# Performance work log

Hardware: AMD Instinct MI355X
Metric: run time of the kernel (lower is better)

## Reference

```python
import jax, jax.numpy as jnp
import numpy as np

EPS = 1e-06
ITERS = 10


def _dilate(x):
    # 3x3 max-pool, stride 1, same padding; torch pads max_pool with -inf
    return jax.lax.reduce_window(x, -jnp.inf, jax.lax.max,
                                 (1, 1, 3, 3), (1, 1, 1, 1), 'SAME')


def _erode(x):
    return -_dilate(-x)


def _soft_skeletonize(img, iters=ITERS):
    skel = jnp.zeros_like(img)
    for _ in range(iters):
        opened = _dilate(_erode(img))
        delta = jax.nn.relu(img - opened)
        skel = skel + jax.nn.relu(delta - skel)
        img = _erode(img)
    return skel


def setup_inputs() -> dict:
    key = jax.random.key(0)
    k1, k2 = jax.random.split(key)
    pred_prob = jax.random.normal(k1, (32, 1, 1024, 1024), dtype=jnp.float32)
    gt_onehot = jax.random.uniform(k2, (32, 1, 1024, 1024), dtype=jnp.float32)
    return {"pred_prob": pred_prob, "gt_onehot": gt_onehot}


def reference(pred_prob, gt_onehot):
    # binary branch: C == 1, logits -> sigmoid
    p = jax.nn.sigmoid(pred_prob)
    skel_pred = _soft_skeletonize(p, ITERS)
    skel_gt = _soft_skeletonize(gt_onehot, ITERS)
    tprec = jnp.sum(skel_pred * gt_onehot, axis=(2, 3)) / (jnp.sum(skel_pred, axis=(2, 3)) + EPS)
    tsens = jnp.sum(skel_gt * p, axis=(2, 3)) / (jnp.sum(skel_gt, axis=(2, 3)) + EPS)
    cldice = 2 * tprec * tsens / (tprec + tsens + EPS)
    return 1.0 - jnp.mean(cldice)
```

## Files before the change

### kernel.cpp

```cpp
#include <hip/hip_runtime.h>
#include <math.h>


typedef unsigned int u32;
typedef _Float16 h2 __attribute__((ext_vector_type(2)));

#define STRD 52
#define BB   0x7BFF7BFFu
#define NB   0xFBFFFBFFu

__device__ __forceinline__ u32 ab(u32 hi, u32 lo) {
  return __builtin_amdgcn_alignbit(hi, lo, 16);
}
__device__ __forceinline__ u32 bcu(h2 x) { return __builtin_bit_cast(u32, x); }
__device__ __forceinline__ h2  bch(u32 x) { return __builtin_bit_cast(h2, x); }
__device__ __forceinline__ u32 pmin(u32 a, u32 b) {
  return bcu(__builtin_elementwise_min(bch(a), bch(b)));
}
__device__ __forceinline__ u32 pmax(u32 a, u32 b) {
  return bcu(__builtin_elementwise_max(bch(a), bch(b)));
}
__device__ __forceinline__ u32 pmin3(u32 a, u32 b, u32 c) { return pmin(pmin(a, b), c); }
__device__ __forceinline__ u32 pmax3(u32 a, u32 b, u32 c) { return pmax(pmax(a, b), c); }
__device__ __forceinline__ u32 skup(u32 sk, u32 im, u32 op) {
  h2 d = bch(im) - bch(op);
  return bcu(__builtin_elementwise_max(bch(sk), d));
}
__device__ __forceinline__ float sigmoidf_(float x) {
  return 1.0f / (1.0f + __expf(-x));
}

__device__ __forceinline__ void load12(const u32* __restrict__ p,
                                       u32* __restrict__ r) {
  uint4 a = *(const uint4*)p;
  uint4 b = *(const uint4*)(p + 4);
  uint4 c = *(const uint4*)(p + 8);
  r[0]=a.x; r[1]=a.y; r[2]=a.z; r[3]=a.w;
  r[4]=b.x; r[5]=b.y; r[6]=b.z; r[7]=b.w;
  r[8]=c.x; r[9]=c.y; r[10]=c.z; r[11]=c.w;
}

__device__ __forceinline__ void store12(u32* __restrict__ q,
                                        const u32* __restrict__ r) {
  *(uint4*)(q)     = make_uint4(r[0], r[1], r[2],  r[3]);
  *(uint4*)(q + 4) = make_uint4(r[4], r[5], r[6],  r[7]);
  *(uint4*)(q + 8) = make_uint4(r[8], r[9], r[10], r[11]);
}

__device__ __forceinline__ void hrow12(const u32* __restrict__ v,
                                       u32 hl, u32 hr,
                                       u32* __restrict__ o) {
  u32 m0 = ab(v[0], hl);
  #pragma unroll
  for (int i = 0; i < 12; ++i) {
    u32 m1 = (i < 11) ? ab(v[i + 1], v[i]) : ab(hr, v[11]);
    o[i] = pmin3(m0, v[i], m1);
    m0 = m1;
  }
}

template <bool FIRST>
__device__ __forceinline__ void erode_compute(
    const u32* __restrict__ E,
    int as3, int eoff, int pu, int pd, bool c0, bool c3,
    u32* __restrict__ e0, u32* __restrict__ e1, u32* __restrict__ e2)
{
  const u32* pr = E + (as3 - 1) * STRD + eoff;
  u32 rT[12], rB[12];
  load12(pr, rT);
  if (FIRST) {
    load12(pr + STRD,     e0);
    load12(pr + 2 * STRD, e1);
    load12(pr + 3 * STRD, e2);
  }
  load12(pr + 4 * STRD, rB);
  u32 t[12], v0[12], v1[12], v2[12];
  #pragma unroll
  for (int i = 0; i < 12; ++i) t[i]  = pmin(e0[i], e1[i]);
  #pragma unroll
  for (int i = 0; i < 12; ++i) v0[i] = pmin(rT[i], t[i]);
  #pragma unroll
  for (int i = 0; i < 12; ++i) v1[i] = pmin(t[i], e2[i]);
  #pragma unroll
  for (int i = 0; i < 12; ++i) v2[i] = pmin(e1[i], pmin(e2[i], rB[i]));
  u32 hl0 = (u32)__builtin_amdgcn_ds_bpermute(pu, (int)v0[11]);
  u32 hr0 = (u32)__builtin_amdgcn_ds_bpermute(pd, (int)v0[0]);
  u32 hl1 = (u32)__builtin_amdgcn_ds_bpermute(pu, (int)v1[11]);
  u32 hr1 = (u32)__builtin_amdgcn_ds_bpermute(pd, (int)v1[0]);
  u32 hl2 = (u32)__builtin_amdgcn_ds_bpermute(pu, (int)v2[11]);
  u32 hr2 = (u32)__builtin_amdgcn_ds_bpermute(pd, (int)v2[0]);
  hl0 = c0 ? BB : hl0;  hr0 = c3 ? BB : hr0;
  hl1 = c0 ? BB : hl1;  hr1 = c3 ? BB : hr1;
  hl2 = c0 ? BB : hl2;  hr2 = c3 ? BB : hr2;
  hrow12(v0, hl0, hr0, e0);
  hrow12(v1, hl1, hr1, e1);
  hrow12(v2, hl2, hr2, e2);
}

__device__ __forceinline__ void erode_store(
    u32* __restrict__ E, int as3, int eoff,
    const u32* __restrict__ e0, const u32* __restrict__ e1,
    const u32* __restrict__ e2)
{
  u32* qw = E + as3 * STRD + eoff;
  store12(qw,            e0);
  store12(qw + STRD,     e1);
  store12(qw + 2 * STRD, e2);
}

__device__ __forceinline__ void dilate_phase(
    const u32* __restrict__ E, const u32* __restrict__ NBR,
    int dr, int db, bool bu, bool bd, bool lfix, bool rfix,
    u32* __restrict__ img, u32* __restrict__ sk)
{
  const u32* pm = bu ? (E + (dr - 1) * STRD + db) : (NBR + db);
  const u32* pc = E + dr * STRD + db;
  const u32* pp = bd ? (E + (dr + 1) * STRD + db) : (NBR + db);
  u32 vm[21];
  #pragma unroll
  for (int j = 0; j < 6; ++j) {
    uint4 x = *(const uint4*)(pm + 4 * j);
    uint4 y = *(const uint4*)(pc + 4 * j);
    uint4 z = *(const uint4*)(pp + 4 * j);
    u32 xs[4] = {x.x, x.y, x.z, x.w};
    u32 ys[4] = {y.x, y.y, y.z, y.w};
    u32 zs[4] = {z.x, z.y, z.z, z.w};
    #pragma unroll
    for (int k = 0; k < 4; ++k) {
      int i = 4 * j + k;
      if (i >= 3 && i <= 20) vm[i] = pmax3(xs[k], ys[k], zs[k]);
    }
  }
  if (lfix) vm[3]  = (vm[3]  & 0x0000FFFFu) | 0xFBFF0000u;
  if (rfix) vm[20] = (vm[20] & 0xFFFF0000u) | 0x0000FBFFu;
  u32 m0 = ab(vm[4], vm[3]);
  #pragma unroll
  for (int j = 0; j < 4; ++j) {
    const uint4 y = *(const uint4*)(pc + 4 + 4 * j);
    const u32 yk[4] = {y.x, y.y, y.z, y.w};
    #pragma unroll
    for (int k = 0; k < 4; ++k) {
      const int i = 4 * j + k;
      u32 m1 = ab(vm[i + 5], vm[i + 4]);
      u32 op = pmax3(m0, vm[i + 4], m1);
      m0 = m1;
      sk[i] = skup(sk[i], img[i], op);
      img[i] = yk[k];
    }
  }
}

__global__ __launch_bounds__(256, 5) void skel_tile_kernel(
    const float* __restrict__ pred, const float* __restrict__ gt,
    float* __restrict__ sums)
{
  __shared__ __align__(16) u32 L[STRD * 97];
  u32* const E = L;
  const u32* const NBR = L + STRD * 96;

  const int tile = blockIdx.x;
  const int b    = blockIdx.y;
  const int s    = blockIdx.z;
  const int txI = tile & 15, tyI = tile >> 4;
  const int x0 = txI * 64 - 16, y0 = tyI * 64 - 16;
  const int t  = threadIdx.x;
  const size_t base = (size_t)b << 20;
  const float* __restrict__ src  = s ? gt   : pred;
  const float* __restrict__ osrc = s ? pred : gt;

  for (int i = t; i < STRD; i += 256) L[STRD * 96 + i] = NB;

  for (int i = t; i < 86 * 12; i += 256) {
    int ci = i % 12, row = i / 12 + 5;
    int gy = y0 + row, gx0 = x0 + ci * 8;
    uint4 hv;
    if ((unsigned)gy < 1024u && gx0 >= 0 && gx0 + 8 <= 1024) {
      const size_t g = base + (size_t)gy * 1024 + gx0;
      const float4 f0 = *(const float4*)&src[g];
      const float4 f1 = *(const float4*)&src[g + 4];
      float ff[8] = {f0.x, f0.y, f0.z, f0.w, f1.x, f1.y, f1.z, f1.w};
      u32 d[4];
      #pragma unroll
      for (int e = 0; e < 4; ++e) {
        float a = ff[2 * e], bb2 = ff[2 * e + 1];
        if (s == 0) { a = sigmoidf_(a); bb2 = sigmoidf_(bb2); }
        h2 p; p[0] = (_Float16)a; p[1] = (_Float16)bb2;
        d[e] = bcu(p);
      }
      hv = make_uint4(d[0], d[1], d[2], d[3]);
    } else {
      u32 d[4];
      #pragma unroll
      for (int e = 0; e < 4; ++e) {
        float va = 65504.0f, vb = 65504.0f;
        int gxa = gx0 + 2 * e, gxb = gxa + 1;
        if ((unsigned)gy < 1024u && (unsigned)gxa < 1024u) {
          va = src[base + (size_t)gy * 1024 + gxa];
          if (s == 0) va = sigmoidf_(va);
        }
        if ((unsigned)gy < 1024u && (unsigned)gxb < 1024u) {
          vb = src[base + (size_t)gy * 1024 + gxb];
          if (s == 0) vb = sigmoidf_(vb);
        }
        h2 p; p[0] = (_Float16)va; p[1] = (_Float16)vb;
        d[e] = bcu(p);
      }
      hv = make_uint4(d[0], d[1], d[2], d[3]);
    }
    *(uint4*)&E[row * STRD + ci * 4] = hv;
  }
  __syncthreads();

  const int lane = t & 63, wid = t >> 6;

  const int seg = t >> 2, ec = t & 3;
  const int as3 = 3 * seg;
  const bool c0 = (ec == 0), c3 = (ec == 3);
  const int pu = ((lane - 1) & 63) * 4;
  const int pd = ((lane + 1) & 63) * 4;
  const int eoff = 12 * ec;

  const int q  = wid - 2;
  const int dr = 16 + lane;
  const int db = 4 + 16 * q;
  const int gyD = y0 + dr;
  const bool bu = (gyD >= 1), bd = (gyD <= 1022);
  const bool lfix = (q == 0) && (txI == 0);
  const bool rfix = (q == 1) && (txI == 15);

  u32 st[36];
  u32* const e0 = st;
  u32* const e1 = st + 12;
  u32* const e2 = st + 24;
  u32* const img = st;
  u32* const sk  = st + 16;

  const bool a0 = !(as3 + 2 < 6 || as3 > 89);
  if (wid < 2) {
    if (a0) erode_compute<true>(E, as3, eoff, pu, pd, c0, c3, e0, e1, e2);
  } else {
    #pragma unroll
    for (int i = 0; i < 16; ++i) sk[i] = 0;
    const u32* p = E + dr * STRD + db;
    #pragma unroll
    for (int i = 0; i < 4; ++i) {
      uint4 v = *(const uint4*)(p + 4 + 4 * i);
      img[4*i] = v.x; img[4*i+1] = v.y; img[4*i+2] = v.z; img[4*i+3] = v.w;
    }
  }
  __syncthreads();
  if (wid < 2 && a0) erode_store(E, as3, eoff, e0, e1, e2);
  __syncthreads();

  #pragma unroll 1
  for (int it = 1; it <= 10; ++it) {
    const bool act = (it < 10) && !(as3 + 2 < 6 + it || as3 > 89 - it);
    if (wid < 2) {
      if (act) erode_compute<false>(E, as3, eoff, pu, pd, c0, c3, e0, e1, e2);
    } else {
      dilate_phase(E, NBR, dr, db, bu, bd, lfix, rfix, img, sk);
    }
    __syncthreads();
    if (wid < 2 && act) erode_store(E, as3, eoff, e0, e1, e2);
    __syncthreads();
  }

  float s0 = 0.f, s1 = 0.f;
  if (wid >= 2) {
    const int gxb = x0 + 2 * db + 8;
    const size_t g = base + (size_t)gyD * 1024 + gxb;
    #pragma unroll
    for (int v4i = 0; v4i < 8; ++v4i) {
      const float4 f = *(const float4*)&osrc[g + 4 * v4i];
      float o0 = f.x, o1 = f.y, o2 = f.z, o3 = f.w;
      if (s == 1) {
        o0 = sigmoidf_(o0); o1 = sigmoidf_(o1);
        o2 = sigmoidf_(o2); o3 = sigmoidf_(o3);
      }
      h2 qa = bch(sk[2 * v4i]);
      h2 qb = bch(sk[2 * v4i + 1]);
      float a0 = (float)qa[0], a1 = (float)qa[1];
      float a2 = (float)qb[0], a3 = (float)qb[1];
      s0 += a0 * o0 + a1 * o1 + a2 * o2 + a3 * o3;
      s1 += a0 + a1 + a2 + a3;
    }
  }
  for (int off = 32; off >= 1; off >>= 1) {
    s0 += __shfl_down(s0, off, 64);
    s1 += __shfl_down(s1, off, 64);
  }
  float* red = (float*)L;
  if (lane == 0) { red[wid * 2] = s0; red[wid * 2 + 1] = s1; }
  __syncthreads();
  if (t == 0) {
    atomicAdd(&sums[(s * 32 + b) * 2 + 0], red[4] + red[6]);
    atomicAdd(&sums[(s * 32 + b) * 2 + 1], red[5] + red[7]);
  }
}

__global__ void finalize_kernel(const float* __restrict__ sums,
                                float* __restrict__ out)
{
  const int t = threadIdx.x;
  float cl = 0.f;
  if (t < 32) {
    float pn = sums[t * 2 + 0],        pd = sums[t * 2 + 1];
    float sn = sums[(32 + t) * 2 + 0], sd = sums[(32 + t) * 2 + 1];
    float tprec = pn / (pd + 1e-6f);
    float tsens = sn / (sd + 1e-6f);
    cl = 2.f * tprec * tsens / (tprec + tsens + 1e-6f);
  }
  for (int off = 32; off >= 1; off >>= 1) cl += __shfl_down(cl, off, 64);
  if (t == 0) out[0] = 1.f - cl / 32.f;
}

extern "C" void kernel_launch(void* const* d_in, const int* in_sizes, int n_in,
                              void* d_out, int out_size, void* d_ws, size_t ws_size,
                              hipStream_t stream) {
  const float* pred = (const float*)d_in[0];
  const float* gt   = (const float*)d_in[1];
  float* sums = (float*)d_ws;
  hipMemsetAsync(sums, 0, 128 * sizeof(float), stream);
  dim3 grid(256, 32, 2);
  skel_tile_kernel<<<grid, dim3(256), 0, stream>>>(pred, gt, sums);
  finalize_kernel<<<1, 64, 0, stream>>>(sums, (float*)d_out);
}
```

Baseline: 647.0 us.

## Split erosion across three wavefronts with two rows per thread, peel final dilate

Adds a third erosion wavefront (320 threads per block) so each erode thread handles 2 rows instead of 3. This shortens the per-iteration erosion critical path that the dilate wavefronts wait on at each barrier. The final dilate pass is peeled out of the loop so the last iteration skips two barriers. The cost is more threads per block and possibly fewer resident blocks, and the reduction indices shift to the new dilate wavefronts.

After: 808.9 us. +25.0%, slower.

```diff
diff --git a/kernel.cpp b/kernel.cpp
--- a/kernel.cpp
+++ b/kernel.cpp
@@ -62,50 +62,41 @@
 template <bool FIRST>
 __device__ __forceinline__ void erode_compute(
     const u32* __restrict__ E,
-    int as3, int eoff, int pu, int pd, bool c0, bool c3,
-    u32* __restrict__ e0, u32* __restrict__ e1, u32* __restrict__ e2)
-{
-  const u32* pr = E + (as3 - 1) * STRD + eoff;
+    int as2, int eoff, int pu, int pd, bool c0, bool c3,
+    u32* __restrict__ e0, u32* __restrict__ e1)
+{
+  const u32* pr = E + (as2 - 1) * STRD + eoff;
   u32 rT[12], rB[12];
   load12(pr, rT);
   if (FIRST) {
     load12(pr + STRD,     e0);
     load12(pr + 2 * STRD, e1);
-    load12(pr + 3 * STRD, e2);
-  }
-  load12(pr + 4 * STRD, rB);
-  u32 t[12], v0[12], v1[12], v2[12];
-  #pragma unroll
-  for (int i = 0; i < 12; ++i) t[i]  = pmin(e0[i], e1[i]);
-  #pragma unroll
-  for (int i = 0; i < 12; ++i) v0[i] = pmin(rT[i], t[i]);
-  #pragma unroll
-  for (int i = 0; i < 12; ++i) v1[i] = pmin(t[i], e2[i]);
-  #pragma unroll
-  for (int i = 0; i < 12; ++i) v2[i] = pmin(e1[i], pmin(e2[i], rB[i]));
+  }
+  load12(pr + 3 * STRD, rB);
+  u32 tt[12], v0[12], v1[12];
+  #pragma unroll
+  for (int i = 0; i < 12; ++i) tt[i] = pmin(e0[i], e1[i]);
+  #pragma unroll
+  for (int i = 0; i < 12; ++i) v0[i] = pmin(rT[i], tt[i]);
+  #pragma unroll
+  for (int i = 0; i < 12; ++i) v1[i] = pmin(tt[i], rB[i]);
   u32 hl0 = (u32)__builtin_amdgcn_ds_bpermute(pu, (int)v0[11]);
   u32 hr0 = (u32)__builtin_amdgcn_ds_bpermute(pd, (int)v0[0]);
   u32 hl1 = (u32)__builtin_amdgcn_ds_bpermute(pu, (int)v1[11]);
   u32 hr1 = (u32)__builtin_amdgcn_ds_bpermute(pd, (int)v1[0]);
-  u32 hl2 = (u32)__builtin_amdgcn_ds_bpermute(pu, (int)v2[11]);
-  u32 hr2 = (u32)__builtin_amdgcn_ds_bpermute(pd, (int)v2[0]);
   hl0 = c0 ? BB : hl0;  hr0 = c3 ? BB : hr0;
   hl1 = c0 ? BB : hl1;  hr1 = c3 ? BB : hr1;
-  hl2 = c0 ? BB : hl2;  hr2 = c3 ? BB : hr2;
   hrow12(v0, hl0, hr0, e0);
   hrow12(v1, hl1, hr1, e1);
-  hrow12(v2, hl2, hr2, e2);
 }
 
 __device__ __forceinline__ void erode_store(
-    u32* __restrict__ E, int as3, int eoff,
-    const u32* __restrict__ e0, const u32* __restrict__ e1,
-    const u32* __restrict__ e2)
-{
-  u32* qw = E + as3 * STRD + eoff;
-  store12(qw,            e0);
-  store12(qw + STRD,     e1);
-  store12(qw + 2 * STRD, e2);
+    u32* __restrict__ E, int as2, int eoff,
+    const u32* __restrict__ e0, const u32* __restrict__ e1)
+{
+  u32* qw = E + as2 * STRD + eoff;
+  store12(qw,        e0);
+  store12(qw + STRD, e1);
 }
 
 __device__ __forceinline__ void dilate_phase(
@@ -150,7 +141,7 @@
   }
 }
 
-__global__ __launch_bounds__(256, 5) void skel_tile_kernel(
+__global__ __launch_bounds__(320, 5) void skel_tile_kernel(
     const float* __restrict__ pred, const float* __restrict__ gt,
     float* __restrict__ sums)
 {
@@ -168,9 +159,9 @@
   const float* __restrict__ src  = s ? gt   : pred;
   const float* __restrict__ osrc = s ? pred : gt;
 
-  for (int i = t; i < STRD; i += 256) L[STRD * 96 + i] = NB;
-
-  for (int i = t; i < 86 * 12; i += 256) {
+  for (int i = t; i < STRD; i += 320) L[STRD * 96 + i] = NB;
+
+  for (int i = t; i < 86 * 12; i += 320) {
     int ci = i % 12, row = i / 12 + 5;
     int gy = y0 + row, gx0 = x0 + ci * 8;
     uint4 hv;
@@ -214,13 +205,13 @@
   const int lane = t & 63, wid = t >> 6;
 
   const int seg = t >> 2, ec = t & 3;
-  const int as3 = 3 * seg;
+  const int as2 = 2 * seg;
   const bool c0 = (ec == 0), c3 = (ec == 3);
   const int pu = ((lane - 1) & 63) * 4;
   const int pd = ((lane + 1) & 63) * 4;
   const int eoff = 12 * ec;
 
-  const int q  = wid - 2;
+  const int q  = wid - 3;
   const int dr = 16 + lane;
   const int db = 4 + 16 * q;
   const int gyD = y0 + dr;
@@ -228,16 +219,15 @@
   const bool lfix = (q == 0) && (txI == 0);
   const bool rfix = (q == 1) && (txI == 15);
 
-  u32 st[36];
+  u32 st[32];
   u32* const e0 = st;
   u32* const e1 = st + 12;
-  u32* const e2 = st + 24;
   u32* const img = st;
   u32* const sk  = st + 16;
 
-  const bool a0 = !(as3 + 2 < 6 || as3 > 89);
-  if (wid < 2) {
-    if (a0) erode_compute<true>(E, as3, eoff, pu, pd, c0, c3, e0, e1, e2);
+  const bool a0 = !(as2 + 1 < 6 || as2 > 89);
+  if (wid < 3) {
+    if (a0) erode_compute<true>(E, as2, eoff, pu, pd, c0, c3, e0, e1);
   } else {
     #pragma unroll
     for (int i = 0; i < 16; ++i) sk[i] = 0;
@@ -249,24 +239,28 @@
     }
   }
   __syncthreads();
-  if (wid < 2 && a0) erode_store(E, as3, eoff, e0, e1, e2);
+  if (wid < 3 && a0) erode_store(E, as2, eoff, e0, e1);
   __syncthreads();
 
   #pragma unroll 1
-  for (int it = 1; it <= 10; ++it) {
-    const bool act = (it < 10) && !(as3 + 2 < 6 + it || as3 > 89 - it);
-    if (wid < 2) {
-      if (act) erode_compute<false>(E, as3, eoff, pu, pd, c0, c3, e0, e1, e2);
+  for (int it = 1; it <= 9; ++it) {
+    const bool act = !(as2 + 1 < 6 + it || as2 > 89 - it);
+    if (wid < 3) {
+      if (act) erode_compute<false>(E, as2, eoff, pu, pd, c0, c3, e0, e1);
     } else {
       dilate_phase(E, NBR, dr, db, bu, bd, lfix, rfix, img, sk);
     }
     __syncthreads();
-    if (wid < 2 && act) erode_store(E, as3, eoff, e0, e1, e2);
+    if (wid < 3 && act) erode_store(E, as2, eoff, e0, e1);
     __syncthreads();
   }
 
+  if (wid >= 3) {
+    dilate_phase(E, NBR, dr, db, bu, bd, lfix, rfix, img, sk);
+  }
+
   float s0 = 0.f, s1 = 0.f;
-  if (wid >= 2) {
+  if (wid >= 3) {
     const int gxb = x0 + 2 * db + 8;
     const size_t g = base + (size_t)gyD * 1024 + gxb;
     #pragma unroll
@@ -293,8 +287,8 @@
   if (lane == 0) { red[wid * 2] = s0; red[wid * 2 + 1] = s1; }
   __syncthreads();
   if (t == 0) {
-    atomicAdd(&sums[(s * 32 + b) * 2 + 0], red[4] + red[6]);
-    atomicAdd(&sums[(s * 32 + b) * 2 + 1], red[5] + red[7]);
+    atomicAdd(&sums[(s * 32 + b) * 2 + 0], red[6] + red[8]);
+    atomicAdd(&sums[(s * 32 + b) * 2 + 1], red[7] + red[9]);
   }
 }
 
@@ -322,6 +316,6 @@
   float* sums = (float*)d_ws;
   hipMemsetAsync(sums, 0, 128 * sizeof(float), stream);
   dim3 grid(256, 32, 2);
-  skel_tile_kernel<<<grid, dim3(256), 0, stream>>>(pred, gt, sums);
+  skel_tile_kernel<<<grid, dim3(320), 0, stream>>>(pred, gt, sums);
   finalize_kernel<<<1, 64, 0, stream>>>(sums, (float*)d_out);
 }
```
